# Performance work log

Hardware: AMD Instinct MI355X
Metric: run time of the kernel (lower is better)

## Reference

```python
import jax, jax.numpy as jnp
import numpy as np

N_POINTS = 131072
N_ANCHORS = 2048


def setup_inputs() -> dict:
    key = jax.random.key(0)
    k1, k2, k3, k4 = jax.random.split(key, 4)
    locations3d = jax.random.normal(k1, (N_POINTS, 3), dtype=jnp.float32)
    anchor_locations3d = jax.random.normal(k2, (N_ANCHORS, 3), dtype=jnp.float32)
    anchor_coeffs = jax.random.normal(k3, (N_ANCHORS,), dtype=jnp.float32)
    # per-anchor widths, kept strictly positive in [0.1, 1.0)
    anchor_parameters = jax.random.uniform(k4, (N_ANCHORS,), dtype=jnp.float32) * 0.9 + 0.1
    return {
        "locations3d": locations3d,
        "anchor_locations3d": anchor_locations3d,
        "anchor_coeffs": anchor_coeffs,
        "anchor_parameters": anchor_parameters,
    }


def potential_operator(locations3d, anchor_locations3d, anchor_parameters):
    # Pairwise squared distances via the expanded form (avoids [N,M,3] intermediate):
    x_sq = jnp.sum(locations3d * locations3d, axis=-1, keepdims=True)          # [N,1]
    a_sq = jnp.sum(anchor_locations3d * anchor_locations3d, axis=-1)            # [M]
    cross = locations3d @ anchor_locations3d.T                                  # [N,M]
    sqdist = x_sq + a_sq[None, :] - 2.0 * cross
    sqdist = jnp.maximum(sqdist, 0.0)
    inv_two_w2 = 0.5 / (anchor_parameters * anchor_parameters)                  # [M]
    return jnp.exp(-sqdist * inv_two_w2[None, :])                               # [N,M]


def reference(locations3d, anchor_locations3d, anchor_coeffs, anchor_parameters):
    K = potential_operator(locations3d, anchor_locations3d, anchor_parameters)  # [N,M]
    return K @ anchor_coeffs                                                    # [N]
```

## Files before the change

### kernel.cpp

```cpp
#include <hip/hip_runtime.h>

#define N_POINTS  131072
#define N_ANCHORS 2048
#define THREADS   256
#define PTS_BLK   128
#define NBLOCKS   (N_POINTS / PTS_BLK)
#define NTILES_M  (N_ANCHORS / 16)
#define LOG2E     1.4426950408889634f

typedef __attribute__((ext_vector_type(8))) short  short8;
typedef __attribute__((ext_vector_type(4))) float  f32x4;


static __device__ __forceinline__ unsigned short f2bf(float v) {
    union { float f; unsigned u; } c; c.f = v;
    unsigned r = (c.u + 0x7FFFu + ((c.u >> 16) & 1u)) >> 16;
    return (unsigned short)r;
}
static __device__ __forceinline__ float bf2f(unsigned short h) {
    union { unsigned u; float f; } c; c.u = ((unsigned)h) << 16;
    return c.f;
}
static __device__ __forceinline__ void split3(float v, unsigned short& h1,
                                              unsigned short& h2, unsigned short& h3) {
    h1 = f2bf(v); float v2 = v - bf2f(h1);
    h2 = f2bf(v2); float v3 = v2 - bf2f(h2);
    h3 = f2bf(v3);
}

#define BF_ONE ((short)0x3F80)

__global__ void prep_B(const float* __restrict__ aloc,
                       const float* __restrict__ coeffs,
                       const float* __restrict__ params,
                       short8* __restrict__ Bws,
                       float* __restrict__ cfws) {
    const int gid  = blockIdx.x * blockDim.x + threadIdx.x;
    const int tile = gid >> 6;
    const int lane = gid & 63;
    const int kb   = lane >> 4;
    const int m    = tile * 16 + (lane & 15);

    const float a0 = aloc[3 * m + 0];
    const float a1 = aloc[3 * m + 1];
    const float a2 = aloc[3 * m + 2];
    const float w  = params[m];
    const float sp = -(0.5f * LOG2E) / (w * w);
    const float r0 = -2.0f * sp * a0;
    const float r1 = -2.0f * sp * a1;
    const float r2 = -2.0f * sp * a2;
    const float q  = sp * (a0 * a0 + a1 * a1 + a2 * a2);

    unsigned short r0a, r0b, r0c, r1a, r1b, r1c, r2a, r2b, r2c, spa, spb, spc, qa, qb, qc;
    split3(r0, r0a, r0b, r0c);
    split3(r1, r1a, r1b, r1c);
    split3(r2, r2a, r2b, r2c);
    split3(sp, spa, spb, spc);
    split3(q,  qa,  qb,  qc);

    short8 fr;
    switch (kb) {
    case 0: fr = (short8){(short)r0a,(short)r0b,(short)r0a,(short)r0c,(short)r0a,(short)r0b,(short)r1a,(short)r1b}; break;
    case 1: fr = (short8){(short)r1a,(short)r1c,(short)r1a,(short)r1b,(short)r2a,(short)r2b,(short)r2a,(short)r2c}; break;
    case 2: fr = (short8){(short)r2a,(short)r2b,(short)spa,(short)spb,(short)spa,(short)spc,(short)spa,(short)spb}; break;
    default:fr = (short8){(short)qa, (short)qb, (short)qc, 0, 0, 0, 0, 0}; break;
    }
    Bws[tile * 64 + lane] = fr;

    if (lane < 16) cfws[m] = coeffs[m];
}

__global__ __launch_bounds__(256, 4) void lp_main(
    const float* __restrict__ xloc,
    const short8* __restrict__ Bws,
    const float* __restrict__ cfws,
    float* __restrict__ out)
{
    __shared__ short8 sA[8][64];

    const int t = threadIdx.x;

    #pragma unroll
    for (int e0 = 0; e0 < 2; ++e0) {
        const int e    = t + e0 * 256;
        const int tl   = e >> 6;
        const int lane = e & 63;
        const int kb   = lane >> 4;
        const int p    = blockIdx.x * PTS_BLK + tl * 16 + (lane & 15);

        const float x = xloc[3 * p + 0];
        const float y = xloc[3 * p + 1];
        const float z = xloc[3 * p + 2];
        const float ss = fmaf(x, x, fmaf(y, y, z * z));

        unsigned short xa, xb, xc, ya, yb, yc, za, zb, zc, sa, sb, sc;
        split3(x,  xa, xb, xc);
        split3(y,  ya, yb, yc);
        split3(z,  za, zb, zc);
        split3(ss, sa, sb, sc);

        short8 fr;
        switch (kb) {
        case 0: fr = (short8){(short)xa,(short)xa,(short)xb,(short)xa,(short)xc,(short)xb,(short)ya,(short)ya}; break;
        case 1: fr = (short8){(short)yb,(short)ya,(short)yc,(short)yb,(short)za,(short)za,(short)zb,(short)za}; break;
        case 2: fr = (short8){(short)zc,(short)zb,(short)sa,(short)sa,(short)sb,(short)sa,(short)sc,(short)sb}; break;
        default:fr = (short8){BF_ONE, BF_ONE, BF_ONE, 0, 0, 0, 0, 0}; break;
        }
        sA[tl][lane] = fr;
    }
    __syncthreads();

    const int wave = t >> 6;
    const int lane = t & 63;
    const int col  = lane & 15;

    const short8 a0 = sA[wave * 2 + 0][lane];
    const short8 a1 = sA[wave * 2 + 1][lane];

    f32x4 acc0 = {0.f, 0.f, 0.f, 0.f};
    f32x4 acc1 = {0.f, 0.f, 0.f, 0.f};
    const f32x4 cz = {0.f, 0.f, 0.f, 0.f};

    #pragma unroll 2
    for (int tm = 0; tm < NTILES_M; ++tm) {
        const short8 bf = Bws[tm * 64 + lane];
        const float  cf = cfws[tm * 16 + col];

        f32x4 c0 = __builtin_amdgcn_mfma_f32_16x16x32_bf16(a0, bf, cz, 0, 0, 0);
        f32x4 c1 = __builtin_amdgcn_mfma_f32_16x16x32_bf16(a1, bf, cz, 0, 0, 0);

        #pragma unroll
        for (int r = 0; r < 4; ++r) {
            acc0[r] = fmaf(cf, __builtin_amdgcn_exp2f(c0[r]), acc0[r]);
            acc1[r] = fmaf(cf, __builtin_amdgcn_exp2f(c1[r]), acc1[r]);
        }
    }

    #pragma unroll
    for (int o = 1; o < 16; o <<= 1) {
        #pragma unroll
        for (int r = 0; r < 4; ++r) {
            acc0[r] += __shfl_xor(acc0[r], o, 16);
            acc1[r] += __shfl_xor(acc1[r], o, 16);
        }
    }

    if (col == 0) {
        const int kb = lane >> 4;
        const int pb = blockIdx.x * PTS_BLK + wave * 32;
        #pragma unroll
        for (int r = 0; r < 4; ++r) {
            out[pb +      kb * 4 + r] = acc0[r];
            out[pb + 16 + kb * 4 + r] = acc1[r];
        }
    }
}

extern "C" void kernel_launch(void* const* d_in, const int* in_sizes, int n_in,
                              void* d_out, int out_size, void* d_ws, size_t ws_size,
                              hipStream_t stream) {
    const float* xloc   = (const float*)d_in[0];
    const float* aloc   = (const float*)d_in[1];
    const float* coeffs = (const float*)d_in[2];
    const float* params = (const float*)d_in[3];
    float* out = (float*)d_out;

    short8* Bws = (short8*)d_ws;
    float*  cfws = (float*)((char*)d_ws + NTILES_M * 64 * sizeof(short8));

    prep_B<<<dim3((NTILES_M * 64) / THREADS), dim3(THREADS), 0, stream>>>(
        aloc, coeffs, params, Bws, cfws);

    lp_main<<<dim3(NBLOCKS), dim3(THREADS), 0, stream>>>(
        xloc, Bws, cfws, out);
}
```

Baseline: 92.41 us.

## Use one 16-point tile per wave and build A fragments in registers

Each wave now handles a single 16-point MFMA tile instead of two, which halves the points per block and doubles the grid. Each lane builds its A fragment directly from global memory, so the shared-memory staging and the barrier are gone. The launch-bounds occupancy hint is raised to 8 blocks per CU. The trade-off is that every B fragment and coefficient load from global or L2 now feeds one MFMA instead of two, so B traffic per point doubles and there is less independent work per iteration to hide the exp2 latency.

```diff
diff --git a/kernel.cpp b/kernel.cpp
--- a/kernel.cpp
+++ b/kernel.cpp
@@ -3,7 +3,7 @@
 #define N_POINTS  131072
 #define N_ANCHORS 2048
 #define THREADS   256
-#define PTS_BLK   128
+#define PTS_BLK   64
 #define NBLOCKS   (N_POINTS / PTS_BLK)
 #define NTILES_M  (N_ANCHORS / 16)
 #define LOG2E     1.4426950408889634f
@@ -70,55 +70,39 @@
     if (lane < 16) cfws[m] = coeffs[m];
 }
 
-__global__ __launch_bounds__(256, 4) void lp_main(
+__global__ __launch_bounds__(256, 8) void lp_main(
     const float* __restrict__ xloc,
     const short8* __restrict__ Bws,
     const float* __restrict__ cfws,
     float* __restrict__ out)
 {
-    __shared__ short8 sA[8][64];
-
-    const int t = threadIdx.x;
-
-    #pragma unroll
-    for (int e0 = 0; e0 < 2; ++e0) {
-        const int e    = t + e0 * 256;
-        const int tl   = e >> 6;
-        const int lane = e & 63;
-        const int kb   = lane >> 4;
-        const int p    = blockIdx.x * PTS_BLK + tl * 16 + (lane & 15);
-
-        const float x = xloc[3 * p + 0];
-        const float y = xloc[3 * p + 1];
-        const float z = xloc[3 * p + 2];
-        const float ss = fmaf(x, x, fmaf(y, y, z * z));
-
-        unsigned short xa, xb, xc, ya, yb, yc, za, zb, zc, sa, sb, sc;
-        split3(x,  xa, xb, xc);
-        split3(y,  ya, yb, yc);
-        split3(z,  za, zb, zc);
-        split3(ss, sa, sb, sc);
-
-        short8 fr;
-        switch (kb) {
-        case 0: fr = (short8){(short)xa,(short)xa,(short)xb,(short)xa,(short)xc,(short)xb,(short)ya,(short)ya}; break;
-        case 1: fr = (short8){(short)yb,(short)ya,(short)yc,(short)yb,(short)za,(short)za,(short)zb,(short)za}; break;
-        case 2: fr = (short8){(short)zc,(short)zb,(short)sa,(short)sa,(short)sb,(short)sa,(short)sc,(short)sb}; break;
-        default:fr = (short8){BF_ONE, BF_ONE, BF_ONE, 0, 0, 0, 0, 0}; break;
-        }
-        sA[tl][lane] = fr;
-    }
-    __syncthreads();
-
+    const int t    = threadIdx.x;
     const int wave = t >> 6;
     const int lane = t & 63;
     const int col  = lane & 15;
+    const int kb   = lane >> 4;
 
-    const short8 a0 = sA[wave * 2 + 0][lane];
-    const short8 a1 = sA[wave * 2 + 1][lane];
+    const int p = blockIdx.x * PTS_BLK + wave * 16 + col;
+    const float x = xloc[3 * p + 0];
+    const float y = xloc[3 * p + 1];
+    const float z = xloc[3 * p + 2];
+    const float ss = fmaf(x, x, fmaf(y, y, z * z));
 
-    f32x4 acc0 = {0.f, 0.f, 0.f, 0.f};
-    f32x4 acc1 = {0.f, 0.f, 0.f, 0.f};
+    unsigned short xa, xb, xc, ya, yb, yc, za, zb, zc, sa, sb, sc;
+    split3(x,  xa, xb, xc);
+    split3(y,  ya, yb, yc);
+    split3(z,  za, zb, zc);
+    split3(ss, sa, sb, sc);
+
+    short8 af;
+    switch (kb) {
+    case 0: af = (short8){(short)xa,(short)xa,(short)xb,(short)xa,(short)xc,(short)xb,(short)ya,(short)ya}; break;
+    case 1: af = (short8){(short)yb,(short)ya,(short)yc,(short)yb,(short)za,(short)za,(short)zb,(short)za}; break;
+    case 2: af = (short8){(short)zc,(short)zb,(short)sa,(short)sa,(short)sb,(short)sa,(short)sc,(short)sb}; break;
+    default:af = (short8){BF_ONE, BF_ONE, BF_ONE, 0, 0, 0, 0, 0}; break;
+    }
+
+    f32x4 acc = {0.f, 0.f, 0.f, 0.f};
     const f32x4 cz = {0.f, 0.f, 0.f, 0.f};
 
     #pragma unroll 2
@@ -126,33 +110,25 @@
         const short8 bf = Bws[tm * 64 + lane];
         const float  cf = cfws[tm * 16 + col];
 
-        f32x4 c0 = __builtin_amdgcn_mfma_f32_16x16x32_bf16(a0, bf, cz, 0, 0, 0);
-        f32x4 c1 = __builtin_amdgcn_mfma_f32_16x16x32_bf16(a1, bf, cz, 0, 0, 0);
+        f32x4 c = __builtin_amdgcn_mfma_f32_16x16x32_bf16(af, bf, cz, 0, 0, 0);
 
         #pragma unroll
-        for (int r = 0; r < 4; ++r) {
-            acc0[r] = fmaf(cf, __builtin_amdgcn_exp2f(c0[r]), acc0[r]);
-            acc1[r] = fmaf(cf, __builtin_amdgcn_exp2f(c1[r]), acc1[r]);
-        }
+        for (int r = 0; r < 4; ++r)
+            acc[r] = fmaf(cf, __builtin_amdgcn_exp2f(c[r]), acc[r]);
     }
 
     #pragma unroll
     for (int o = 1; o < 16; o <<= 1) {
         #pragma unroll
-        for (int r = 0; r < 4; ++r) {
-            acc0[r] += __shfl_xor(acc0[r], o, 16);
-            acc1[r] += __shfl_xor(acc1[r], o, 16);
-        }
+        for (int r = 0; r < 4; ++r)
+            acc[r] += __shfl_xor(acc[r], o, 16);
     }
 
     if (col == 0) {
-        const int kb = lane >> 4;
-        const int pb = blockIdx.x * PTS_BLK + wave * 32;
+        const int pb = blockIdx.x * PTS_BLK + wave * 16 + kb * 4;
         #pragma unroll
-        for (int r = 0; r < 4; ++r) {
-            out[pb +      kb * 4 + r] = acc0[r];
-            out[pb + 16 + kb * 4 + r] = acc1[r];
-        }
+        for (int r = 0; r < 4; ++r)
+            out[pb + r] = acc[r];
     }
 }
 
```

Result: slower. 100.8 us (+9.0%).

## Split anchors into chunks with register-resident B tiles and add partial-sum reduction

Applied to the files above, without the earlier changes.

The main kernel now uses a 2D grid. Each block handles 512 points and one of 8 anchor chunks. Each wave preloads its 16 anchor tiles and coefficients into registers and reuses them across 8 point tiles, which removes the per-iteration global loads of B. Partial sums are written to workspace, and a new kernel adds the 8 chunks together. In exchange this adds register pressure, an extra launch, and global traffic for the partials.

```diff
diff --git a/kernel.cpp b/kernel.cpp
--- a/kernel.cpp
+++ b/kernel.cpp
@@ -3,9 +3,11 @@
 #define N_POINTS  131072
 #define N_ANCHORS 2048
 #define THREADS   256
-#define PTS_BLK   128
-#define NBLOCKS   (N_POINTS / PTS_BLK)
+#define PTS_BLK   512
+#define NBX       (N_POINTS / PTS_BLK)
+#define MCHUNKS   8
 #define NTILES_M  (N_ANCHORS / 16)
+#define TILES_CH  (NTILES_M / MCHUNKS)
 #define LOG2E     1.4426950408889634f
 
 typedef __attribute__((ext_vector_type(8))) short  short8;
@@ -74,14 +76,14 @@
     const float* __restrict__ xloc,
     const short8* __restrict__ Bws,
     const float* __restrict__ cfws,
-    float* __restrict__ out)
+    float* __restrict__ part)
 {
-    __shared__ short8 sA[8][64];
+    __shared__ short8 sA[32][64];
 
     const int t = threadIdx.x;
 
     #pragma unroll
-    for (int e0 = 0; e0 < 2; ++e0) {
+    for (int e0 = 0; e0 < 8; ++e0) {
         const int e    = t + e0 * 256;
         const int tl   = e >> 6;
         const int lane = e & 63;
@@ -108,52 +110,67 @@
         }
         sA[tl][lane] = fr;
     }
-    __syncthreads();
 
     const int wave = t >> 6;
     const int lane = t & 63;
     const int col  = lane & 15;
+    const int kb   = lane >> 4;
 
-    const short8 a0 = sA[wave * 2 + 0][lane];
-    const short8 a1 = sA[wave * 2 + 1][lane];
+    const int tm0 = blockIdx.y * TILES_CH;
+    short8 breg[TILES_CH];
+    float  cfr[TILES_CH];
+    #pragma unroll
+    for (int k = 0; k < TILES_CH; ++k) {
+        breg[k] = Bws[(tm0 + k) * 64 + lane];
+        cfr[k]  = cfws[(tm0 + k) * 16 + col];
+    }
 
-    f32x4 acc0 = {0.f, 0.f, 0.f, 0.f};
-    f32x4 acc1 = {0.f, 0.f, 0.f, 0.f};
+    __syncthreads();
+
     const f32x4 cz = {0.f, 0.f, 0.f, 0.f};
+    float* __restrict__ pchunk = part + (size_t)blockIdx.y * N_POINTS;
 
-    #pragma unroll 2
-    for (int tm = 0; tm < NTILES_M; ++tm) {
-        const short8 bf = Bws[tm * 64 + lane];
-        const float  cf = cfws[tm * 16 + col];
+    #pragma unroll 1
+    for (int pt = 0; pt < 8; ++pt) {
+        const int tl = wave * 8 + pt;
+        const short8 af = sA[tl][lane];
 
-        f32x4 c0 = __builtin_amdgcn_mfma_f32_16x16x32_bf16(a0, bf, cz, 0, 0, 0);
-        f32x4 c1 = __builtin_amdgcn_mfma_f32_16x16x32_bf16(a1, bf, cz, 0, 0, 0);
+        f32x4 acc = {0.f, 0.f, 0.f, 0.f};
 
         #pragma unroll
-        for (int r = 0; r < 4; ++r) {
-            acc0[r] = fmaf(cf, __builtin_amdgcn_exp2f(c0[r]), acc0[r]);
-            acc1[r] = fmaf(cf, __builtin_amdgcn_exp2f(c1[r]), acc1[r]);
+        for (int k = 0; k < TILES_CH; ++k) {
+            f32x4 c = __builtin_amdgcn_mfma_f32_16x16x32_bf16(af, breg[k], cz, 0, 0, 0);
+            #pragma unroll
+            for (int r = 0; r < 4; ++r)
+                acc[r] = fmaf(cfr[k], __builtin_amdgcn_exp2f(c[r]), acc[r]);
+        }
+
+        #pragma unroll
+        for (int o = 1; o < 16; o <<= 1) {
+            #pragma unroll
+            for (int r = 0; r < 4; ++r)
+                acc[r] += __shfl_xor(acc[r], o, 16);
+        }
+
+        if (col == 0) {
+            const int pb = blockIdx.x * PTS_BLK + tl * 16 + kb * 4;
+            #pragma unroll
+            for (int r = 0; r < 4; ++r)
+                pchunk[pb + r] = acc[r];
         }
     }
+}
 
+__global__ void reduce_parts(const float4* __restrict__ part4,
+                             float4* __restrict__ out4) {
+    const int i = blockIdx.x * blockDim.x + threadIdx.x;
+    float4 s = part4[i];
     #pragma unroll
-    for (int o = 1; o < 16; o <<= 1) {
-        #pragma unroll
-        for (int r = 0; r < 4; ++r) {
-            acc0[r] += __shfl_xor(acc0[r], o, 16);
-            acc1[r] += __shfl_xor(acc1[r], o, 16);
-        }
+    for (int c = 1; c < MCHUNKS; ++c) {
+        const float4 p = part4[c * (N_POINTS / 4) + i];
+        s.x += p.x; s.y += p.y; s.z += p.z; s.w += p.w;
     }
-
-    if (col == 0) {
-        const int kb = lane >> 4;
-        const int pb = blockIdx.x * PTS_BLK + wave * 32;
-        #pragma unroll
-        for (int r = 0; r < 4; ++r) {
-            out[pb +      kb * 4 + r] = acc0[r];
-            out[pb + 16 + kb * 4 + r] = acc1[r];
-        }
-    }
+    out4[i] = s;
 }
 
 extern "C" void kernel_launch(void* const* d_in, const int* in_sizes, int n_in,
@@ -165,12 +182,16 @@
     const float* params = (const float*)d_in[3];
     float* out = (float*)d_out;
 
-    short8* Bws = (short8*)d_ws;
-    float*  cfws = (float*)((char*)d_ws + NTILES_M * 64 * sizeof(short8));
+    short8* Bws  = (short8*)d_ws;
+    float*  cfws = (float*)((char*)d_ws + 128 * 1024);
+    float*  part = (float*)((char*)d_ws + 256 * 1024);
 
-    prep_B<<<dim3((NTILES_M * 64) / THREADS), dim3(THREADS), 0, stream>>>(
+    prep_B<<<dim3((NTILES_M * 64) / 256), dim3(256), 0, stream>>>(
         aloc, coeffs, params, Bws, cfws);
 
-    lp_main<<<dim3(NBLOCKS), dim3(THREADS), 0, stream>>>(
-        xloc, Bws, cfws, out);
+    lp_main<<<dim3(NBX, MCHUNKS), dim3(THREADS), 0, stream>>>(
+        xloc, Bws, cfws, part);
+
+    reduce_parts<<<dim3(N_POINTS / 4 / 256), dim3(256), 0, stream>>>(
+        (const float4*)part, (float4*)out);
 }
```

Measured after the change: 116.1 us. +25.6%, slower.
